# Kernel optimization log

Measured on AMD Instinct MI355X. Metric: run time of the kernel, lower is better.

Reference implementation:

```python
import jax, jax.numpy as jnp
import numpy as np

WEIGHT = 1.0
SIM_THRESHOLD = 0.8


def setup_inputs() -> dict:
    key = jax.random.key(0)
    k1, k2, k3, k4 = jax.random.split(key, 4)
    B, E, H, C = 8192, 16, 1024, 128  # batch, num_experts, hidden, clusters
    routing_probs = jax.random.normal(k1, (B, E), dtype=jnp.float32)
    # Clustered embeddings so some pairs exceed the similarity threshold:
    # intra-cluster cosine sim ~ 1024/(1024 + 0.09*1024) ~ 0.92 > 0.8.
    centers = jax.random.normal(k2, (C, H), dtype=jnp.float32)
    assign = jax.random.randint(k3, (B,), 0, C)
    input_embeddings = centers[assign] + 0.3 * jax.random.normal(k4, (B, H), dtype=jnp.float32)
    return {"routing_probs": routing_probs, "input_embeddings": input_embeddings}


def reference(routing_probs, input_embeddings):
    B = routing_probs.shape[0]
    # L2-normalize embeddings and build pairwise cosine similarity [B, B]
    emb = input_embeddings / jnp.linalg.norm(input_embeddings, axis=-1, keepdims=True)
    sim = emb @ emb.T
    mask = (sim > SIM_THRESHOLD) & ~jnp.eye(B, dtype=bool)
    # Batch-wide softmax/log_softmax computed once (fuses the per-pair loop)
    L = jax.nn.log_softmax(routing_probs, axis=-1)  # [B, E]
    P = jnp.exp(L)                                   # [B, E]
    neg_entropy = jnp.sum(P * L, axis=-1)            # [B], sum_k p_j log p_j
    # kl[i, j] = KL(P_j || P_i) = sum_k P_j (log P_j - L_i)
    kl = neg_entropy[None, :] - L @ P.T              # [B, B]
    cnt = jnp.sum(mask)
    loss = jnp.where(
        cnt > 0,
        jnp.sum(jnp.where(mask, kl, 0.0)) / jnp.maximum(cnt, 1).astype(kl.dtype),
        jnp.array(0.0, dtype=kl.dtype),
    )
    return WEIGHT * loss
```

## Files before the change

kernel.cpp:

```cpp
#include <hip/hip_runtime.h>
#include <hip/hip_bf16.h>
#include <math.h>

#define B_SZ 8192
#define H_SZ 1024
#define E_SZ 16
#define SIM_THR_I 12903
typedef float floatx4 __attribute__((ext_vector_type(4)));
typedef int   intx4   __attribute__((ext_vector_type(4)));

#define OFF_NE   4096
#define OFF_L    65536
#define OFF_P    (65536 + 524288)
#define OFF_EMB  2097152


__device__ __forceinline__ void gload16(const void* g, void* l) {
    __builtin_amdgcn_global_load_lds(
        (const __attribute__((address_space(1))) void*)g,
        (__attribute__((address_space(3))) void*)l, 16, 0, 0);
}

__device__ __forceinline__ unsigned int pack4_i8(float4 v, float s) {
    int a = (int)rintf(v.x * s), b = (int)rintf(v.y * s);
    int c = (int)rintf(v.z * s), d = (int)rintf(v.w * s);
    return (a & 255) | ((b & 255) << 8) | ((c & 255) << 16) | ((d & 255) << 24);
}

__global__ __launch_bounds__(256)
void prep_kernel(const float* __restrict__ rp,
                 const float* __restrict__ emb,
                 unsigned char* __restrict__ out8,
                 float* __restrict__ L, float* __restrict__ P,
                 float* __restrict__ ne,
                 float* __restrict__ gsum, unsigned int* __restrict__ gcnt,
                 unsigned int* __restrict__ done) {
    const int b = blockIdx.x;
    const int tid = threadIdx.x;
    if (b < 512) {
        __shared__ __align__(16) unsigned char stage[16 * 1040];
        const int wave = tid >> 6, lane = tid & 63;
        const int g = b;
#pragma unroll
        for (int t = 0; t < 4; t++) {
            int r = g * 16 + wave * 4 + t;
            const float4* row4 = (const float4*)(emb + (size_t)r * H_SZ);
            float4 v0 = row4[lane * 4 + 0], v1 = row4[lane * 4 + 1];
            float4 v2 = row4[lane * 4 + 2], v3 = row4[lane * 4 + 3];
            float ss = v0.x*v0.x + v0.y*v0.y + v0.z*v0.z + v0.w*v0.w
                     + v1.x*v1.x + v1.y*v1.y + v1.z*v1.z + v1.w*v1.w
                     + v2.x*v2.x + v2.y*v2.y + v2.z*v2.z + v2.w*v2.w
                     + v3.x*v3.x + v3.y*v3.y + v3.z*v3.z + v3.w*v3.w;
#pragma unroll
            for (int off = 32; off > 0; off >>= 1) ss += __shfl_down(ss, off, 64);
            ss = __shfl(ss, 0, 64);
            float s = rsqrtf(ss) * 127.0f;
            uint4 c;
            c.x = pack4_i8(v0, s);
            c.y = pack4_i8(v1, s);
            c.z = pack4_i8(v2, s);
            c.w = pack4_i8(v3, s);
            *(uint4*)(stage + (r & 15) * 1040 + lane * 16) = c;
        }
        __syncthreads();
#pragma unroll
        for (int p = 0; p < 4; p++) {
            int d = p * 256 + tid;
            int m = d & 15;
            int c = (d >> 6) * 4 + ((d >> 4) & 3);
            uint4 v = *(const uint4*)(stage + m * 1040 + c * 16);
            *(uint4*)(out8 + (size_t)g * 16384 + (size_t)d * 16) = v;
        }
    } else {
        int i = (b - 512) * 256 + tid;
        if (i == 0) { *gsum = 0.f; *gcnt = 0u; *done = 0u; }
        if (i >= B_SZ) return;
        const float* x = rp + i * E_SZ;
        float v[E_SZ];
        float m = -INFINITY;
#pragma unroll
        for (int k = 0; k < E_SZ; k++) { v[k] = x[k]; m = fmaxf(m, v[k]); }
        float s = 0.f;
#pragma unroll
        for (int k = 0; k < E_SZ; k++) s += expf(v[k] - m);
        float lse = m + logf(s);
        float nent = 0.f;
#pragma unroll
        for (int k = 0; k < E_SZ; k++) {
            float l = v[k] - lse;
            float p = expf(l);
            L[i * E_SZ + k] = l;
            P[i * E_SZ + k] = p;
            nent += p * l;
        }
        ne[i] = nent;
    }
}

__global__ __launch_bounds__(1024, 4)
void sim_kl_kernel(const unsigned char* __restrict__ embL,
                   const float* __restrict__ Lm, const float* __restrict__ Pm,
                   const float* __restrict__ ne,
                   float* __restrict__ gsum, unsigned int* __restrict__ gcnt,
                   unsigned int* __restrict__ done, float* __restrict__ out) {
    __shared__ __align__(16) char smem[131072];
    __shared__ float redf[16];
    __shared__ unsigned int redc[16];

    const int x = blockIdx.x & 7;
    int s = blockIdx.x >> 3;
    const int phase = s & 15;
    int bjs[4] = { x, x + 8, 23 - x, 31 - x };
    int bi = 0, bj = 0;
#pragma unroll
    for (int t = 0; t < 4; t++) {
        int n = bjs[t] + 1;
        if (s < n) { bj = bjs[t]; bi = s; break; }
        s -= n;
    }
    const int rowI = bi * 256, rowJ = bj * 256;

    const int tid  = threadIdx.x;
    const int lane = tid & 63;
    const int wave = tid >> 6;
    const int wrg = wave >> 2;
    const int wcg = wave & 3;
    const int quad = lane >> 4;
    const int l16  = lane & 15;

    intx4 acc[4][4];
#pragma unroll
    for (int mi = 0; mi < 4; mi++)
#pragma unroll
        for (int ni = 0; ni < 4; ni++) {
            intx4 z = {0, 0, 0, 0};
            acc[mi][ni] = z;
        }

    const char* srcA = (const char*)embL + (size_t)(bi * 16 + wave) * 16384 + lane * 16;
    const char* srcB = (const char*)embL + (size_t)(bj * 16 + wave) * 16384 + lane * 16;
    const int gW = wave * 1024;

#pragma unroll
    for (int p = 0; p < 3; p++) {
        const int ko = ((p + phase) & 15) * 1024;
        gload16(srcA + ko, smem + p * 16384 + gW);
        gload16(srcB + ko, smem + 65536 + p * 16384 + gW);
    }

    const int aoff = wrg * 4096 + lane * 16;
    const int boff = 65536 + wcg * 4096 + lane * 16;

#pragma unroll
    for (int kt = 0; kt < 16; kt++) {
        if (kt < 14)
            asm volatile("s_waitcnt vmcnt(4)\ns_barrier" ::: "memory");
        else if (kt == 14)
            asm volatile("s_waitcnt vmcnt(2)\ns_barrier" ::: "memory");
        else
            asm volatile("s_waitcnt vmcnt(0)\ns_barrier" ::: "memory");

        const int slot = kt & 3;
        intx4 af[4], bf[4];
#pragma unroll
        for (int mi = 0; mi < 4; mi++)
            af[mi] = *(const intx4*)(smem + slot * 16384 + aoff + mi * 1024);
#pragma unroll
        for (int ni = 0; ni < 4; ni++)
            bf[ni] = *(const intx4*)(smem + slot * 16384 + boff + ni * 1024);
#pragma unroll
        for (int mi = 0; mi < 4; mi++)
#pragma unroll
            for (int ni = 0; ni < 4; ni++)
                acc[mi][ni] = __builtin_amdgcn_mfma_i32_16x16x64_i8(
                    af[mi], bf[ni], acc[mi][ni], 0, 0, 0);

        if (kt + 3 < 16) {
            const int ko = ((kt + 3 + phase) & 15) * 1024;
            const int ps = (kt + 3) & 3;
            gload16(srcA + ko, smem + ps * 16384 + gW);
            gload16(srcB + ko, smem + 65536 + ps * 16384 + gW);
        }
    }

    __syncthreads();
    unsigned short* wl = (unsigned short*)smem + wave * 2048;
    int base = 0;
#pragma unroll
    for (int mi = 0; mi < 4; mi++) {
#pragma unroll
        for (int ni = 0; ni < 4; ni++) {
#pragma unroll
            for (int r = 0; r < 4; r++) {
                int il = wrg * 64 + mi * 16 + quad * 4 + r;
                int jl = wcg * 64 + ni * 16 + l16;
                bool msk = (acc[mi][ni][r] > SIM_THR_I) && (rowJ + jl > rowI + il);
                unsigned long long bal = __ballot(msk);
                if (msk) {
                    int pos = base + __popcll(bal & ((1ull << lane) - 1ull));
                    if (pos < 2048) wl[pos] = (unsigned short)((il << 8) | jl);
                }
                base += __popcll(bal);
            }
        }
    }
    if (base > 2048) base = 2048;

    float fsum = 0.f;
    unsigned int lcnt = 0;
    for (int t = lane; t < base; t += 64) {
        int e = wl[t];
        int i = rowI + (e >> 8), j = rowJ + (e & 255);
        const float4* Li4 = (const float4*)(Lm + i * E_SZ);
        const float4* Pj4 = (const float4*)(Pm + j * E_SZ);
        const float4* Lj4 = (const float4*)(Lm + j * E_SZ);
        const float4* Pi4 = (const float4*)(Pm + i * E_SZ);
        float d = 0.f, d2 = 0.f;
#pragma unroll
        for (int q = 0; q < 4; q++) {
            float4 a = Li4[q], bb = Pj4[q];
            d += a.x * bb.x + a.y * bb.y + a.z * bb.z + a.w * bb.w;
            float4 a2 = Lj4[q], b2 = Pi4[q];
            d2 += a2.x * b2.x + a2.y * b2.y + a2.z * b2.z + a2.w * b2.w;
        }
        fsum += (ne[j] - d) + (ne[i] - d2);
        lcnt += 2;
    }

#pragma unroll
    for (int off = 32; off > 0; off >>= 1) {
        fsum += __shfl_down(fsum, off, 64);
        lcnt += __shfl_down(lcnt, off, 64);
    }
    if (lane == 0) { redf[wave] = fsum; redc[wave] = lcnt; }
    __syncthreads();
    if (tid == 0) {
        float sv = 0.f;
        unsigned int c = 0u;
#pragma unroll
        for (int w = 0; w < 16; w++) { sv += redf[w]; c += redc[w]; }
        if (c > 0u) {
            atomicAdd(gsum, sv);
            atomicAdd(gcnt, c);
        }
        __threadfence();
        unsigned int old = atomicAdd(done, 1u);
        if (old == gridDim.x - 1) {
            float S = atomicAdd(gsum, 0.0f);
            unsigned int C = atomicAdd(gcnt, 0u);
            out[0] = (C > 0u) ? (S / (float)C) : 0.f;
        }
    }
}

extern "C" void kernel_launch(void* const* d_in, const int* in_sizes, int n_in,
                              void* d_out, int out_size, void* d_ws, size_t ws_size,
                              hipStream_t stream) {
    const float* rp  = (const float*)d_in[0];
    const float* emb = (const float*)d_in[1];
    float* out = (float*)d_out;

    char* ws = (char*)d_ws;
    float*         gsum = (float*)(ws + 0);
    unsigned int*  gcnt = (unsigned int*)(ws + 4);
    unsigned int*  done = (unsigned int*)(ws + 8);
    float*         ne   = (float*)(ws + OFF_NE);
    float*         Lm   = (float*)(ws + OFF_L);
    float*         Pm   = (float*)(ws + OFF_P);
    unsigned char* embL = (unsigned char*)(ws + OFF_EMB);

    prep_kernel<<<512 + 32, 256, 0, stream>>>(rp, emb, embL, Lm, Pm, ne, gsum, gcnt, done);
    sim_kl_kernel<<<528, 1024, 0, stream>>>(embL, Lm, Pm, ne, gsum, gcnt, done, out);
}
```

Baseline: 148.3 us.

## Split tail tiles into quarter-blocks to balance the last wave

The 16 leftover 256x256 similarity tiles, which previously ran as a lone partial final wave, are each split into four 128x128 sub-tiles handled by extra blocks. These blocks load int8 fragments straight from global memory into registers with a small register ring instead of staging through LDS. Sub-tiles lying entirely below the diagonal are skipped. The launch bound is relaxed from 4 to 2 blocks per CU, which may change register allocation. The aim is to cut tail-wave imbalance, at the cost of less data reuse in the split blocks.

Result: faster. 144.1 us (-2.8%).

```diff
diff --git a/kernel.cpp b/kernel.cpp
--- a/kernel.cpp
+++ b/kernel.cpp
@@ -97,7 +97,7 @@
     }
 }
 
-__global__ __launch_bounds__(1024, 4)
+__global__ __launch_bounds__(1024, 2)
 void sim_kl_kernel(const unsigned char* __restrict__ embL,
                    const float* __restrict__ Lm, const float* __restrict__ Pm,
                    const float* __restrict__ ne,
@@ -107,124 +107,226 @@
     __shared__ float redf[16];
     __shared__ unsigned int redc[16];
 
-    const int x = blockIdx.x & 7;
-    int s = blockIdx.x >> 3;
-    const int phase = s & 15;
-    int bjs[4] = { x, x + 8, 23 - x, 31 - x };
-    int bi = 0, bj = 0;
-#pragma unroll
-    for (int t = 0; t < 4; t++) {
-        int n = bjs[t] + 1;
-        if (s < n) { bj = bjs[t]; bi = s; break; }
-        s -= n;
-    }
-    const int rowI = bi * 256, rowJ = bj * 256;
-
     const int tid  = threadIdx.x;
     const int lane = tid & 63;
     const int wave = tid >> 6;
-    const int wrg = wave >> 2;
-    const int wcg = wave & 3;
     const int quad = lane >> 4;
     const int l16  = lane & 15;
 
-    intx4 acc[4][4];
-#pragma unroll
-    for (int mi = 0; mi < 4; mi++)
-#pragma unroll
-        for (int ni = 0; ni < 4; ni++) {
-            intx4 z = {0, 0, 0, 0};
-            acc[mi][ni] = z;
-        }
-
-    const char* srcA = (const char*)embL + (size_t)(bi * 16 + wave) * 16384 + lane * 16;
-    const char* srcB = (const char*)embL + (size_t)(bj * 16 + wave) * 16384 + lane * 16;
-    const int gW = wave * 1024;
-
-#pragma unroll
-    for (int p = 0; p < 3; p++) {
-        const int ko = ((p + phase) & 15) * 1024;
-        gload16(srcA + ko, smem + p * 16384 + gW);
-        gload16(srcB + ko, smem + 65536 + p * 16384 + gW);
-    }
-
-    const int aoff = wrg * 4096 + lane * 16;
-    const int boff = 65536 + wcg * 4096 + lane * 16;
-
-#pragma unroll
-    for (int kt = 0; kt < 16; kt++) {
-        if (kt < 14)
-            asm volatile("s_waitcnt vmcnt(4)\ns_barrier" ::: "memory");
-        else if (kt == 14)
-            asm volatile("s_waitcnt vmcnt(2)\ns_barrier" ::: "memory");
-        else
-            asm volatile("s_waitcnt vmcnt(0)\ns_barrier" ::: "memory");
-
-        const int slot = kt & 3;
-        intx4 af[4], bf[4];
-#pragma unroll
-        for (int mi = 0; mi < 4; mi++)
-            af[mi] = *(const intx4*)(smem + slot * 16384 + aoff + mi * 1024);
-#pragma unroll
-        for (int ni = 0; ni < 4; ni++)
-            bf[ni] = *(const intx4*)(smem + slot * 16384 + boff + ni * 1024);
-#pragma unroll
-        for (int mi = 0; mi < 4; mi++)
-#pragma unroll
-            for (int ni = 0; ni < 4; ni++)
-                acc[mi][ni] = __builtin_amdgcn_mfma_i32_16x16x64_i8(
-                    af[mi], bf[ni], acc[mi][ni], 0, 0, 0);
-
-        if (kt + 3 < 16) {
-            const int ko = ((kt + 3 + phase) & 15) * 1024;
-            const int ps = (kt + 3) & 3;
-            gload16(srcA + ko, smem + ps * 16384 + gW);
-            gload16(srcB + ko, smem + 65536 + ps * 16384 + gW);
-        }
-    }
-
-    __syncthreads();
-    unsigned short* wl = (unsigned short*)smem + wave * 2048;
-    int base = 0;
-#pragma unroll
-    for (int mi = 0; mi < 4; mi++) {
-#pragma unroll
-        for (int ni = 0; ni < 4; ni++) {
-#pragma unroll
-            for (int r = 0; r < 4; r++) {
-                int il = wrg * 64 + mi * 16 + quad * 4 + r;
-                int jl = wcg * 64 + ni * 16 + l16;
-                bool msk = (acc[mi][ni][r] > SIM_THR_I) && (rowJ + jl > rowI + il);
-                unsigned long long bal = __ballot(msk);
-                if (msk) {
-                    int pos = base + __popcll(bal & ((1ull << lane) - 1ull));
-                    if (pos < 2048) wl[pos] = (unsigned short)((il << 8) | jl);
-                }
-                base += __popcll(bal);
-            }
-        }
-    }
-    if (base > 2048) base = 2048;
-
     float fsum = 0.f;
     unsigned int lcnt = 0;
-    for (int t = lane; t < base; t += 64) {
-        int e = wl[t];
-        int i = rowI + (e >> 8), j = rowJ + (e & 255);
-        const float4* Li4 = (const float4*)(Lm + i * E_SZ);
-        const float4* Pj4 = (const float4*)(Pm + j * E_SZ);
-        const float4* Lj4 = (const float4*)(Lm + j * E_SZ);
-        const float4* Pi4 = (const float4*)(Pm + i * E_SZ);
-        float d = 0.f, d2 = 0.f;
-#pragma unroll
-        for (int q = 0; q < 4; q++) {
-            float4 a = Li4[q], bb = Pj4[q];
-            d += a.x * bb.x + a.y * bb.y + a.z * bb.z + a.w * bb.w;
-            float4 a2 = Lj4[q], b2 = Pi4[q];
-            d2 += a2.x * b2.x + a2.y * b2.y + a2.z * b2.z + a2.w * b2.w;
-        }
-        fsum += (ne[j] - d) + (ne[i] - d2);
-        lcnt += 2;
+
+    if (blockIdx.x < 512) {
+        const int x = blockIdx.x & 7;
+        int s = blockIdx.x >> 3;
+        const int phase = s & 15;
+        int bjs[4] = { x, x + 8, 23 - x, 31 - x };
+        int bi = 0, bj = 0;
+#pragma unroll
+        for (int t = 0; t < 4; t++) {
+            int n = bjs[t] + 1;
+            if (s < n) { bj = bjs[t]; bi = s; break; }
+            s -= n;
+        }
+        const int rowI = bi * 256, rowJ = bj * 256;
+        const int wrg = wave >> 2;
+        const int wcg = wave & 3;
+
+        intx4 acc[4][4];
+#pragma unroll
+        for (int mi = 0; mi < 4; mi++)
+#pragma unroll
+            for (int ni = 0; ni < 4; ni++) {
+                intx4 z = {0, 0, 0, 0};
+                acc[mi][ni] = z;
+            }
+
+        const char* srcA = (const char*)embL + (size_t)(bi * 16 + wave) * 16384 + lane * 16;
+        const char* srcB = (const char*)embL + (size_t)(bj * 16 + wave) * 16384 + lane * 16;
+        const int gW = wave * 1024;
+
+#pragma unroll
+        for (int p = 0; p < 3; p++) {
+            const int ko = ((p + phase) & 15) * 1024;
+            gload16(srcA + ko, smem + p * 16384 + gW);
+            gload16(srcB + ko, smem + 65536 + p * 16384 + gW);
+        }
+
+        const int aoff = wrg * 4096 + lane * 16;
+        const int boff = 65536 + wcg * 4096 + lane * 16;
+
+#pragma unroll
+        for (int kt = 0; kt < 16; kt++) {
+            if (kt < 14)
+                asm volatile("s_waitcnt vmcnt(4)\ns_barrier" ::: "memory");
+            else if (kt == 14)
+                asm volatile("s_waitcnt vmcnt(2)\ns_barrier" ::: "memory");
+            else
+                asm volatile("s_waitcnt vmcnt(0)\ns_barrier" ::: "memory");
+
+            const int slot = kt & 3;
+            intx4 af[4], bf[4];
+#pragma unroll
+            for (int mi = 0; mi < 4; mi++)
+                af[mi] = *(const intx4*)(smem + slot * 16384 + aoff + mi * 1024);
+#pragma unroll
+            for (int ni = 0; ni < 4; ni++)
+                bf[ni] = *(const intx4*)(smem + slot * 16384 + boff + ni * 1024);
+#pragma unroll
+            for (int mi = 0; mi < 4; mi++)
+#pragma unroll
+                for (int ni = 0; ni < 4; ni++)
+                    acc[mi][ni] = __builtin_amdgcn_mfma_i32_16x16x64_i8(
+                        af[mi], bf[ni], acc[mi][ni], 0, 0, 0);
+
+            if (kt + 3 < 16) {
+                const int ko = ((kt + 3 + phase) & 15) * 1024;
+                const int ps = (kt + 3) & 3;
+                gload16(srcA + ko, smem + ps * 16384 + gW);
+                gload16(srcB + ko, smem + 65536 + ps * 16384 + gW);
+            }
+        }
+
+        __syncthreads();
+        unsigned short* wl = (unsigned short*)smem + wave * 2048;
+        int base = 0;
+#pragma unroll
+        for (int mi = 0; mi < 4; mi++) {
+#pragma unroll
+            for (int ni = 0; ni < 4; ni++) {
+#pragma unroll
+                for (int r = 0; r < 4; r++) {
+                    int il = wrg * 64 + mi * 16 + quad * 4 + r;
+                    int jl = wcg * 64 + ni * 16 + l16;
+                    bool msk = (acc[mi][ni][r] > SIM_THR_I) && (rowJ + jl > rowI + il);
+                    unsigned long long bal = __ballot(msk);
+                    if (msk) {
+                        int pos = base + __popcll(bal & ((1ull << lane) - 1ull));
+                        if (pos < 2048) wl[pos] = (unsigned short)((il << 8) | jl);
+                    }
+                    base += __popcll(bal);
+                }
+            }
+        }
+        if (base > 2048) base = 2048;
+
+        for (int t = lane; t < base; t += 64) {
+            int e = wl[t];
+            int i = rowI + (e >> 8), j = rowJ + (e & 255);
+            const float4* Li4 = (const float4*)(Lm + i * E_SZ);
+            const float4* Pj4 = (const float4*)(Pm + j * E_SZ);
+            const float4* Lj4 = (const float4*)(Lm + j * E_SZ);
+            const float4* Pi4 = (const float4*)(Pm + i * E_SZ);
+            float d = 0.f, d2 = 0.f;
+#pragma unroll
+            for (int q = 0; q < 4; q++) {
+                float4 a = Li4[q], bb = Pj4[q];
+                d += a.x * bb.x + a.y * bb.y + a.z * bb.z + a.w * bb.w;
+                float4 a2 = Lj4[q], b2 = Pi4[q];
+                d2 += a2.x * b2.x + a2.y * b2.y + a2.z * b2.z + a2.w * b2.w;
+            }
+            fsum += (ne[j] - d) + (ne[i] - d2);
+            lcnt += 2;
+        }
+    } else {
+        const int q0 = blockIdx.x - 512;
+        const int x  = q0 & 7;
+        const int e  = q0 >> 3;
+        const int bj = 31 - x;
+        const int bi = 30 - x + (e >> 2);
+        const int h  = (e >> 1) & 1;
+        const int c  = e & 1;
+        const int rowI = bi * 256, rowJ = bj * 256;
+        const int rI0 = rowI + h * 128, rJ0 = rowJ + c * 128;
+
+        intx4 acc[2][2];
+#pragma unroll
+        for (int mi = 0; mi < 2; mi++)
+#pragma unroll
+            for (int ni = 0; ni < 2; ni++) {
+                intx4 z = {0, 0, 0, 0};
+                acc[mi][ni] = z;
+            }
+
+        const bool skip = (rJ0 + 127 <= rI0);
+        if (!skip) {
+            const int wrg = wave >> 2;
+            const int wcg = wave & 3;
+            const char* pA = (const char*)embL
+                + (size_t)(bi * 16 + h * 8 + wrg * 2) * 16384 + lane * 16;
+            const char* pB = (const char*)embL
+                + (size_t)(bj * 16 + c * 8 + wcg * 2) * 16384 + lane * 16;
+
+            intx4 fa[3][2], fb[3][2];
+#pragma unroll
+            for (int p = 0; p < 3; p++)
+#pragma unroll
+                for (int mi = 0; mi < 2; mi++) {
+                    fa[p][mi] = *(const intx4*)(pA + mi * 16384 + p * 1024);
+                    fb[p][mi] = *(const intx4*)(pB + mi * 16384 + p * 1024);
+                }
+#pragma unroll
+            for (int kt = 0; kt < 16; kt++) {
+                const int buf = kt % 3;
+#pragma unroll
+                for (int mi = 0; mi < 2; mi++)
+#pragma unroll
+                    for (int ni = 0; ni < 2; ni++)
+                        acc[mi][ni] = __builtin_amdgcn_mfma_i32_16x16x64_i8(
+                            fa[buf][mi], fb[buf][ni], acc[mi][ni], 0, 0, 0);
+                if (kt + 3 < 16) {
+                    const int ko = (kt + 3) * 1024;
+#pragma unroll
+                    for (int mi = 0; mi < 2; mi++) {
+                        fa[buf][mi] = *(const intx4*)(pA + mi * 16384 + ko);
+                        fb[buf][mi] = *(const intx4*)(pB + mi * 16384 + ko);
+                    }
+                }
+            }
+
+            unsigned short* wl = (unsigned short*)smem + wave * 2048;
+            int base = 0;
+            const int wrl = h * 128 + wrg * 32;
+            const int wcl = c * 128 + wcg * 32;
+#pragma unroll
+            for (int mi = 0; mi < 2; mi++) {
+#pragma unroll
+                for (int ni = 0; ni < 2; ni++) {
+#pragma unroll
+                    for (int r = 0; r < 4; r++) {
+                        int il = wrl + mi * 16 + quad * 4 + r;
+                        int jl = wcl + ni * 16 + l16;
+                        bool msk = (acc[mi][ni][r] > SIM_THR_I) && (rowJ + jl > rowI + il);
+                        unsigned long long bal = __ballot(msk);
+                        if (msk) {
+                            int pos = base + __popcll(bal & ((1ull << lane) - 1ull));
+                            if (pos < 2048) wl[pos] = (unsigned short)((il << 8) | jl);
+                        }
+                        base += __popcll(bal);
+                    }
+                }
+            }
+            if (base > 2048) base = 2048;
+
+            for (int t = lane; t < base; t += 64) {
+                int eidx = wl[t];
+                int i = rowI + (eidx >> 8), j = rowJ + (eidx & 255);
+                const float4* Li4 = (const float4*)(Lm + i * E_SZ);
+                const float4* Pj4 = (const float4*)(Pm + j * E_SZ);
+                const float4* Lj4 = (const float4*)(Lm + j * E_SZ);
+                const float4* Pi4 = (const float4*)(Pm + i * E_SZ);
+                float d = 0.f, d2 = 0.f;
+#pragma unroll
+                for (int q = 0; q < 4; q++) {
+                    float4 a = Li4[q], bb = Pj4[q];
+                    d += a.x * bb.x + a.y * bb.y + a.z * bb.z + a.w * bb.w;
+                    float4 a2 = Lj4[q], b2 = Pi4[q];
+                    d2 += a2.x * b2.x + a2.y * b2.y + a2.z * b2.z + a2.w * b2.w;
+                }
+                fsum += (ne[j] - d) + (ne[i] - d2);
+                lcnt += 2;
+            }
+        }
     }
 
 #pragma unroll
@@ -270,5 +372,5 @@
     unsigned char* embL = (unsigned char*)(ws + OFF_EMB);
 
     prep_kernel<<<512 + 32, 256, 0, stream>>>(rp, emb, embL, Lm, Pm, ne, gsum, gcnt, done);
-    sim_kl_kernel<<<528, 1024, 0, stream>>>(embL, Lm, Pm, ne, gsum, gcnt, done, out);
-}
+    sim_kl_kernel<<<576, 1024, 0, stream>>>(embL, Lm, Pm, ne, gsum, gcnt, done, out);
+}
```
